# Performance work log

Hardware: AMD Instinct MI355X
Metric: run time of the kernel (lower is better)

Reference implementation:

```python
import jax, jax.numpy as jnp
import numpy as np

B, H, L = 8, 256, 16384

def setup_inputs() -> dict:
    key = jax.random.key(0)
    k1, k2, k3 = jax.random.split(key, 3)
    u = jax.random.normal(k1, (B, H, L), dtype=jnp.float32)
    # SSM convolution kernel (H, L); small scale to keep tanh unsaturated
    k = jax.random.normal(k2, (H, L), dtype=jnp.float32) * 0.02
    # D feedthrough parameter (H, H); forward only uses its diagonal via einsum 'hh,bhl->bhl'
    D = jax.random.normal(k3, (H, H), dtype=jnp.float32)
    return {"u": u, "k": k, "D": D}

def reference(u, k, D):
    # circular FFT convolution: y = ifft(fft(u) * fft(k)).real
    u_s = jnp.fft.fft(u, axis=-1)          # (B,H,L) complex64
    k_s = jnp.fft.fft(k, axis=-1)          # (H,L)   complex64
    y = jnp.fft.ifft(u_s * k_s[None], axis=-1).real
    # D feedthrough: einsum 'hh,bhl->bhl' uses only diag(D)
    y = y + jnp.einsum('hh,bhl->bhl', D, u)
    return jnp.tanh(y)
```

## Files before the change

### kernel.cpp

```cpp
#include <hip/hip_runtime.h>
#include <math.h>

#define FFT_N 16384
#define NT 512
#define RPT 32
#define B_DIM 8
#define H_DIM 256

#define REGION 2048
#define RW (REGION + (REGION >> 5))
#define PAD(x) ((x) + ((x) >> 5))

#define WAVE_LDS_FENCE() do {                                   \
    __builtin_amdgcn_sched_barrier(0);                          \
    asm volatile("s_waitcnt lgkmcnt(0)" ::: "memory");          \
    __builtin_amdgcn_sched_barrier(0);                          \
} while (0)

__device__ __forceinline__ float2 cmul(float2 a, float2 b) {
    return make_float2(a.x * b.x - a.y * b.y, a.x * b.y + a.y * b.x);
}
__device__ __forceinline__ float2 cadd(float2 a, float2 b) { return make_float2(a.x + b.x, a.y + b.y); }
__device__ __forceinline__ float2 csub(float2 a, float2 b) { return make_float2(a.x - b.x, a.y - b.y); }
__device__ __forceinline__ float2 mulnegi(float2 z) { return make_float2(z.y, -z.x); }
__device__ __forceinline__ float2 mulposi(float2 z) { return make_float2(-z.y, z.x); }

__device__ __forceinline__ void bfly4(float2& a, float2& b, float2& c, float2& d,
                                      float2 w1, float2 w2, float2 w3) {
    float2 apc = cadd(a, c), amc = csub(a, c);
    float2 bpd = cadd(b, d), bmd = csub(b, d);
    float2 nib = mulnegi(bmd);
    a = cadd(apc, bpd);
    b = cmul(csub(apc, bpd), w2);
    c = cmul(cadd(amc, nib), w1);
    d = cmul(csub(amc, nib), w3);
}
__device__ __forceinline__ void bfly4_nw(float2& a, float2& b, float2& c, float2& d) {
    float2 apc = cadd(a, c), amc = csub(a, c);
    float2 bpd = cadd(b, d), bmd = csub(b, d);
    float2 nib = mulnegi(bmd);
    a = cadd(apc, bpd);
    b = csub(apc, bpd);
    c = cadd(amc, nib);
    d = csub(amc, nib);
}
__device__ __forceinline__ void ibfly4(float2& a, float2& b, float2& c, float2& d,
                                       float2 w1t, float2 w2t) {
    float2 w1 = make_float2(w1t.x, -w1t.y);
    float2 w2 = make_float2(w2t.x, -w2t.y);
    float2 bt = cmul(b, w2), dt = cmul(d, w2);
    float2 A = cadd(a, bt), Bb = csub(a, bt);
    float2 C = cadd(c, dt), Dd = csub(c, dt);
    float2 Cw = cmul(C, w1);
    float2 Dw = mulposi(cmul(Dd, w1));
    a = cadd(A, Cw);  c = csub(A, Cw);
    b = cadd(Bb, Dw); d = csub(Bb, Dw);
}
__device__ __forceinline__ void ibfly4_nw(float2& a, float2& b, float2& c, float2& d) {
    float2 A = cadd(a, b), Bb = csub(a, b);
    float2 C = cadd(c, d), Dd = csub(c, d);
    float2 Dw = mulposi(Dd);
    a = cadd(A, C);  c = csub(A, C);
    b = cadd(Bb, Dw); d = csub(Bb, Dw);
}

__device__ __forceinline__ void fwd_g01(float2 r[RPT], int lp, const float2* __restrict__ tw) {
#pragma unroll
    for (int j0 = 0; j0 < 8; ++j0) {
        const int i = lp + NT * j0;
        bfly4(r[j0], r[j0 + 8], r[j0 + 16], r[j0 + 24], tw[i], tw[2 * i], tw[3 * i]);
    }
    {
        const int ie = lp * 4, io = (lp + NT) * 4;
        const float2 we1 = tw[ie], we2 = tw[2 * ie], we3 = tw[3 * ie];
        const float2 wo1 = tw[io], wo2 = tw[2 * io], wo3 = tw[3 * io];
#pragma unroll
        for (int m = 0; m < 8; ++m) {
            const int g = (m >> 1) * 8 + (m & 1);
            if (g & 1) bfly4(r[g], r[g + 2], r[g + 4], r[g + 6], wo1, wo2, wo3);
            else       bfly4(r[g], r[g + 2], r[g + 4], r[g + 6], we1, we2, we3);
        }
    }
}
__device__ __forceinline__ void inv_g01(float2 r[RPT], int lp, const float2* __restrict__ tw) {
    {
        const int ie = lp * 4, io = (lp + NT) * 4;
        const float2 we1 = tw[ie], we2 = tw[2 * ie];
        const float2 wo1 = tw[io], wo2 = tw[2 * io];
#pragma unroll
        for (int m = 0; m < 8; ++m) {
            const int g = (m >> 1) * 8 + (m & 1);
            if (g & 1) ibfly4(r[g], r[g + 2], r[g + 4], r[g + 6], wo1, wo2);
            else       ibfly4(r[g], r[g + 2], r[g + 4], r[g + 6], we1, we2);
        }
    }
#pragma unroll
    for (int j0 = 0; j0 < 8; ++j0) {
        const int i = lp + NT * j0;
        ibfly4(r[j0], r[j0 + 8], r[j0 + 16], r[j0 + 24], tw[i], tw[2 * i]);
    }
}


__device__ __forceinline__ void fwd_mid(float2 r[RPT], float* ldsx, float* ldsy,
                                        const int t, const int w, const int l,
                                        const float2* __restrict__ tw) {
#pragma unroll
    for (int j = 0; j < RPT; ++j) {
        const int e = t + NT * j;
        const int a = (e >> 11) * RW + PAD(e & 2047);
        ldsx[a] = r[j].x; ldsy[a] = r[j].y;
    }
    __syncthreads();
#pragma unroll
    for (int s = 0; s < 2; ++s)
#pragma unroll
        for (int jj = 0; jj < 16; ++jj) {
            const int a = w * RW + PAD(1024 * s + 64 * jj + l);
            r[16 * s + jj].x = ldsx[a];
            r[16 * s + jj].y = ldsy[a];
        }
#pragma unroll
    for (int j0 = 0; j0 < 4; ++j0) {
        const int i1 = 1024 * j0 + 16 * l;
        const float2 w1 = tw[i1], w2 = tw[2 * i1], w3 = tw[3 * i1];
#pragma unroll
        for (int s = 0; s < 2; ++s)
            bfly4(r[16 * s + j0], r[16 * s + j0 + 4], r[16 * s + j0 + 8], r[16 * s + j0 + 12], w1, w2, w3);
    }
    {
        const int i2 = 64 * l;
        const float2 w1 = tw[i2], w2 = tw[2 * i2], w3 = tw[3 * i2];
#pragma unroll
        for (int s = 0; s < 2; ++s)
#pragma unroll
            for (int g = 0; g < 4; ++g)
                bfly4(r[16 * s + 4 * g], r[16 * s + 4 * g + 1], r[16 * s + 4 * g + 2], r[16 * s + 4 * g + 3], w1, w2, w3);
    }
#pragma unroll
    for (int s = 0; s < 2; ++s)
#pragma unroll
        for (int jj = 0; jj < 16; ++jj) {
            const int a = w * RW + PAD(1024 * s + 64 * jj + l);
            ldsx[a] = r[16 * s + jj].x; ldsy[a] = r[16 * s + jj].y;
        }
    WAVE_LDS_FENCE();
    {
        const int lo = 64 * (l >> 2) + (l & 3);
#pragma unroll
        for (int s = 0; s < 2; ++s)
#pragma unroll
            for (int jj = 0; jj < 16; ++jj) {
                const int a = w * RW + PAD(1024 * s + lo + 4 * jj);
                r[16 * s + jj].x = ldsx[a]; r[16 * s + jj].y = ldsy[a];
            }
    }
#pragma unroll
    for (int j0 = 0; j0 < 4; ++j0) {
        const int i3 = 1024 * j0 + 256 * (l & 3);
        const float2 w1 = tw[i3], w2 = tw[2 * i3], w3 = tw[3 * i3];
#pragma unroll
        for (int s = 0; s < 2; ++s)
            bfly4(r[16 * s + j0], r[16 * s + j0 + 4], r[16 * s + j0 + 8], r[16 * s + j0 + 12], w1, w2, w3);
    }
    {
        const int i4 = 1024 * (l & 3);
        const float2 w1 = tw[i4], w2 = tw[2 * i4], w3 = tw[3 * i4];
#pragma unroll
        for (int s = 0; s < 2; ++s)
#pragma unroll
            for (int g = 0; g < 4; ++g)
                bfly4(r[16 * s + 4 * g], r[16 * s + 4 * g + 1], r[16 * s + 4 * g + 2], r[16 * s + 4 * g + 3], w1, w2, w3);
    }
    {
        const int lo = 64 * (l >> 2) + (l & 3);
#pragma unroll
        for (int s = 0; s < 2; ++s)
#pragma unroll
            for (int jj = 0; jj < 16; ++jj) {
                const int a = w * RW + PAD(1024 * s + lo + 4 * jj);
                ldsx[a] = r[16 * s + jj].x; ldsy[a] = r[16 * s + jj].y;
            }
    }
    WAVE_LDS_FENCE();
#pragma unroll
    for (int s = 0; s < 2; ++s)
#pragma unroll
        for (int jj = 0; jj < 16; ++jj) {
            const int a = w * RW + PAD(1024 * s + 16 * l + jj);
            r[16 * s + jj].x = ldsx[a]; r[16 * s + jj].y = ldsy[a];
        }
#pragma unroll
    for (int s = 0; s < 2; ++s)
#pragma unroll
        for (int g = 0; g < 4; ++g)
            bfly4_nw(r[16 * s + 4 * g], r[16 * s + 4 * g + 1], r[16 * s + 4 * g + 2], r[16 * s + 4 * g + 3]);
}

__device__ __forceinline__ void inv_mid(float2 r[RPT], float* ldsx, float* ldsy,
                                        const int t, const int w, const int l,
                                        const float2* __restrict__ tw) {
#pragma unroll
    for (int s = 0; s < 2; ++s)
#pragma unroll
        for (int g = 0; g < 4; ++g)
            ibfly4_nw(r[16 * s + 4 * g], r[16 * s + 4 * g + 1], r[16 * s + 4 * g + 2], r[16 * s + 4 * g + 3]);
#pragma unroll
    for (int s = 0; s < 2; ++s)
#pragma unroll
        for (int jj = 0; jj < 16; ++jj) {
            const int a = w * RW + PAD(1024 * s + 16 * l + jj);
            ldsx[a] = r[16 * s + jj].x; ldsy[a] = r[16 * s + jj].y;
        }
    WAVE_LDS_FENCE();
    {
        const int lo = 64 * (l >> 2) + (l & 3);
#pragma unroll
        for (int s = 0; s < 2; ++s)
#pragma unroll
            for (int jj = 0; jj < 16; ++jj) {
                const int a = w * RW + PAD(1024 * s + lo + 4 * jj);
                r[16 * s + jj].x = ldsx[a]; r[16 * s + jj].y = ldsy[a];
            }
    }
    {
        const int i4 = 1024 * (l & 3);
        const float2 w1 = tw[i4], w2 = tw[2 * i4];
#pragma unroll
        for (int s = 0; s < 2; ++s)
#pragma unroll
            for (int g = 0; g < 4; ++g)
                ibfly4(r[16 * s + 4 * g], r[16 * s + 4 * g + 1], r[16 * s + 4 * g + 2], r[16 * s + 4 * g + 3], w1, w2);
    }
#pragma unroll
    for (int j0 = 0; j0 < 4; ++j0) {
        const int i3 = 1024 * j0 + 256 * (l & 3);
        const float2 w1 = tw[i3], w2 = tw[2 * i3];
#pragma unroll
        for (int s = 0; s < 2; ++s)
            ibfly4(r[16 * s + j0], r[16 * s + j0 + 4], r[16 * s + j0 + 8], r[16 * s + j0 + 12], w1, w2);
    }
    {
        const int lo = 64 * (l >> 2) + (l & 3);
#pragma unroll
        for (int s = 0; s < 2; ++s)
#pragma unroll
            for (int jj = 0; jj < 16; ++jj) {
                const int a = w * RW + PAD(1024 * s + lo + 4 * jj);
                ldsx[a] = r[16 * s + jj].x; ldsy[a] = r[16 * s + jj].y;
            }
    }
    WAVE_LDS_FENCE();
#pragma unroll
    for (int s = 0; s < 2; ++s)
#pragma unroll
        for (int jj = 0; jj < 16; ++jj) {
            const int a = w * RW + PAD(1024 * s + 64 * jj + l);
            r[16 * s + jj].x = ldsx[a]; r[16 * s + jj].y = ldsy[a];
        }
    {
        const int i2 = 64 * l;
        const float2 w1 = tw[i2], w2 = tw[2 * i2];
#pragma unroll
        for (int s = 0; s < 2; ++s)
#pragma unroll
            for (int g = 0; g < 4; ++g)
                ibfly4(r[16 * s + 4 * g], r[16 * s + 4 * g + 1], r[16 * s + 4 * g + 2], r[16 * s + 4 * g + 3], w1, w2);
    }
#pragma unroll
    for (int j0 = 0; j0 < 4; ++j0) {
        const int i1 = 1024 * j0 + 16 * l;
        const float2 w1 = tw[i1], w2 = tw[2 * i1];
#pragma unroll
        for (int s = 0; s < 2; ++s)
            ibfly4(r[16 * s + j0], r[16 * s + j0 + 4], r[16 * s + j0 + 8], r[16 * s + j0 + 12], w1, w2);
    }
#pragma unroll
    for (int s = 0; s < 2; ++s)
#pragma unroll
        for (int jj = 0; jj < 16; ++jj) {
            const int a = w * RW + PAD(1024 * s + 64 * jj + l);
            ldsx[a] = r[16 * s + jj].x; ldsy[a] = r[16 * s + jj].y;
        }
    __syncthreads();
#pragma unroll
    for (int j = 0; j < RPT; ++j) {
        const int e = t + NT * j;
        const int a = (e >> 11) * RW + PAD(e & 2047);
        r[j].x = ldsx[a]; r[j].y = ldsy[a];
    }
}

__device__ __forceinline__ float ftanh(float x) {
    float e = __expf(2.0f * x);
    return 1.0f - 2.0f * __builtin_amdgcn_rcpf(e + 1.0f);
}

__global__ void twiddle_init(float2* __restrict__ tw) {
    int t = blockIdx.x * blockDim.x + threadIdx.x;
    if (t < FFT_N) {
        float ang = -2.0f * 3.14159265358979323846f * (float)t / (float)FFT_N;
        float sv, cv;
        sincosf(ang, &sv, &cv);
        tw[t] = make_float2(cv, sv);
    }
}

__global__ __launch_bounds__(NT)
__attribute__((amdgpu_waves_per_eu(2, 2)))
void kfft_kernel(const float* __restrict__ k,
                 const float* __restrict__ D,
                 const float2* __restrict__ tw,
                 float2* __restrict__ Kf) {
    __shared__ float ldsx[8 * RW];
    __shared__ float ldsy[8 * RW];
    const int h = blockIdx.x;
    const int t = threadIdx.x;
    const int w = t >> 6, l = t & 63;
    const float* krow = k + (size_t)h * FFT_N;
    float2 r[RPT];
#pragma unroll
    for (int j = 0; j < RPT; ++j) r[j] = make_float2(krow[t + NT * j], 0.f);
    if (t == 0) r[0].x += D[h * (H_DIM + 1)];
    fwd_g01(r, t, tw);
    fwd_mid(r, ldsx, ldsy, t, w, l, tw);
    float4* out4 = (float4*)(Kf + (size_t)h * FFT_N);
#pragma unroll
    for (int m = 0; m < 16; ++m)
        out4[16 * t + m] = make_float4(r[2 * m].x, r[2 * m].y, r[2 * m + 1].x, r[2 * m + 1].y);
}

__global__ __launch_bounds__(NT)
__attribute__((amdgpu_waves_per_eu(2, 2)))
void conv_kernel(const float* __restrict__ u,
                 const float2* __restrict__ tw,
                 const float2* __restrict__ Kf,
                 float* __restrict__ out) {
    __shared__ float ldsx[8 * RW];
    __shared__ float ldsy[8 * RW];
    const int raw = blockIdx.x;
    const int vb = ((raw & 7) << 7) + (raw >> 3);
    const int h = vb >> 2;
    const int p = vb & 3;
    const int t = threadIdx.x;
    const int w = t >> 6, l = t & 63;
    const size_t row0 = ((size_t)(2 * p) * H_DIM + h) * FFT_N;
    const size_t row1 = row0 + (size_t)H_DIM * FFT_N;
    const float* u0 = u + row0;
    const float* u1 = u + row1;

    float2 r[RPT];
#pragma unroll
    for (int j = 0; j < RPT; ++j) {
        const int n = t + NT * j;
        r[j] = make_float2(u0[n], u1[n]);
    }

    fwd_g01(r, t, tw);
    fwd_mid(r, ldsx, ldsy, t, w, l, tw);

    {
        const float4* kf4 = (const float4*)(Kf + (size_t)h * FFT_N);
        const float invN = 1.0f / (float)FFT_N;
#pragma unroll
        for (int m = 0; m < 16; ++m) {
            const float4 q = kf4[16 * t + m];
            const float2 z0 = r[2 * m], z1 = r[2 * m + 1];
            r[2 * m]     = make_float2((z0.x * q.x - z0.y * q.y) * invN,
                                       (z0.x * q.y + z0.y * q.x) * invN);
            r[2 * m + 1] = make_float2((z1.x * q.z - z1.y * q.w) * invN,
                                       (z1.x * q.w + z1.y * q.z) * invN);
        }
    }

    inv_mid(r, ldsx, ldsy, t, w, l, tw);
    inv_g01(r, t, tw);

    float* o0 = out + row0;
    float* o1 = out + row1;
#pragma unroll
    for (int j = 0; j < RPT; ++j) {
        const int n = t + NT * j;
        o0[n] = ftanh(r[j].x);
        o1[n] = ftanh(r[j].y);
    }
}

extern "C" void kernel_launch(void* const* d_in, const int* in_sizes, int n_in,
                              void* d_out, int out_size, void* d_ws, size_t ws_size,
                              hipStream_t stream) {
    const float* u = (const float*)d_in[0];
    const float* k = (const float*)d_in[1];
    const float* D = (const float*)d_in[2];
    float* out = (float*)d_out;

    float2* tw = (float2*)d_ws;
    float2* Kf = tw + FFT_N;

    twiddle_init<<<FFT_N / 256, 256, 0, stream>>>(tw);
    kfft_kernel<<<H_DIM, NT, 0, stream>>>(k, D, tw, Kf);
    conv_kernel<<<(B_DIM / 2) * H_DIM, NT, 0, stream>>>(u, tw, Kf, out);
}
```

Before: 199.3 us.

## Split 32-element per-thread FFT state into two 16-element halves to cut registers

Restructures the first two radix-4 stages and the per-wave middle stages so each thread processes two 16-element halves sequentially, spilling the first-stage results to LDS between halves. This lowers live register count and drops the forced waves_per_eu(2,2) attribute, aiming for higher occupancy or fewer spills. It adds extra LDS round trips (inverse first-stage input now read back from LDS) and an extra barrier before the output pass.

After: 224.1 us. 12.4% more time.

```diff
diff --git a/kernel.cpp b/kernel.cpp
--- a/kernel.cpp
+++ b/kernel.cpp
@@ -3,7 +3,6 @@
 
 #define FFT_N 16384
 #define NT 512
-#define RPT 32
 #define B_DIM 8
 #define H_DIM 256
 
@@ -64,230 +63,163 @@
     b = cadd(Bb, Dw); d = csub(Bb, Dw);
 }
 
-__device__ __forceinline__ void fwd_g01(float2 r[RPT], int lp, const float2* __restrict__ tw) {
-#pragma unroll
-    for (int j0 = 0; j0 < 8; ++j0) {
-        const int i = lp + NT * j0;
-        bfly4(r[j0], r[j0 + 8], r[j0 + 16], r[j0 + 24], tw[i], tw[2 * i], tw[3 * i]);
-    }
-    {
-        const int ie = lp * 4, io = (lp + NT) * 4;
-        const float2 we1 = tw[ie], we2 = tw[2 * ie], we3 = tw[3 * ie];
-        const float2 wo1 = tw[io], wo2 = tw[2 * io], wo3 = tw[3 * io];
-#pragma unroll
-        for (int m = 0; m < 8; ++m) {
-            const int g = (m >> 1) * 8 + (m & 1);
-            if (g & 1) bfly4(r[g], r[g + 2], r[g + 4], r[g + 6], wo1, wo2, wo3);
-            else       bfly4(r[g], r[g + 2], r[g + 4], r[g + 6], we1, we2, we3);
-        }
-    }
-}
-__device__ __forceinline__ void inv_g01(float2 r[RPT], int lp, const float2* __restrict__ tw) {
-    {
-        const int ie = lp * 4, io = (lp + NT) * 4;
-        const float2 we1 = tw[ie], we2 = tw[2 * ie];
-        const float2 wo1 = tw[io], wo2 = tw[2 * io];
-#pragma unroll
-        for (int m = 0; m < 8; ++m) {
-            const int g = (m >> 1) * 8 + (m & 1);
-            if (g & 1) ibfly4(r[g], r[g + 2], r[g + 4], r[g + 6], wo1, wo2);
-            else       ibfly4(r[g], r[g + 2], r[g + 4], r[g + 6], we1, we2);
-        }
-    }
-#pragma unroll
-    for (int j0 = 0; j0 < 8; ++j0) {
-        const int i = lp + NT * j0;
-        ibfly4(r[j0], r[j0 + 8], r[j0 + 16], r[j0 + 24], tw[i], tw[2 * i]);
-    }
-}
-
-
-__device__ __forceinline__ void fwd_mid(float2 r[RPT], float* ldsx, float* ldsy,
-                                        const int t, const int w, const int l,
-                                        const float2* __restrict__ tw) {
-#pragma unroll
-    for (int j = 0; j < RPT; ++j) {
-        const int e = t + NT * j;
-        const int a = (e >> 11) * RW + PAD(e & 2047);
-        ldsx[a] = r[j].x; ldsy[a] = r[j].y;
-    }
-    __syncthreads();
-#pragma unroll
-    for (int s = 0; s < 2; ++s)
-#pragma unroll
-        for (int jj = 0; jj < 16; ++jj) {
-            const int a = w * RW + PAD(1024 * s + 64 * jj + l);
-            r[16 * s + jj].x = ldsx[a];
-            r[16 * s + jj].y = ldsy[a];
-        }
+__device__ __forceinline__ void fwd_g01_half(float2 rh[16], const int t, const int par,
+                                             const float2* __restrict__ tw) {
+#pragma unroll
+    for (int m0 = 0; m0 < 4; ++m0) {
+        const int i = t + 512 * par + 1024 * m0;
+        bfly4(rh[m0], rh[m0 + 4], rh[m0 + 8], rh[m0 + 12], tw[i], tw[2 * i], tw[3 * i]);
+    }
+    {
+        const int ig = (t + 512 * par) * 4;
+        const float2 w1 = tw[ig], w2 = tw[2 * ig], w3 = tw[3 * ig];
+#pragma unroll
+        for (int a = 0; a < 4; ++a)
+            bfly4(rh[4 * a], rh[4 * a + 1], rh[4 * a + 2], rh[4 * a + 3], w1, w2, w3);
+    }
+}
+__device__ __forceinline__ void inv_g01_half(float2 rh[16], const int t, const int par,
+                                             const float2* __restrict__ tw) {
+    {
+        const int ig = (t + 512 * par) * 4;
+        const float2 w1 = tw[ig], w2 = tw[2 * ig];
+#pragma unroll
+        for (int a = 0; a < 4; ++a)
+            ibfly4(rh[4 * a], rh[4 * a + 1], rh[4 * a + 2], rh[4 * a + 3], w1, w2);
+    }
+#pragma unroll
+    for (int m0 = 0; m0 < 4; ++m0) {
+        const int i = t + 512 * par + 1024 * m0;
+        ibfly4(rh[m0], rh[m0 + 4], rh[m0 + 8], rh[m0 + 12], tw[i], tw[2 * i]);
+    }
+}
+
+__device__ __forceinline__ void fwd_mid_half(float2 rh[16], float* ldsx, float* ldsy,
+                                             const int w, const int l, const int s,
+                                             const float2* __restrict__ tw) {
+#pragma unroll
+    for (int jj = 0; jj < 16; ++jj) {
+        const int a = w * RW + PAD(1024 * s + 64 * jj + l);
+        rh[jj].x = ldsx[a]; rh[jj].y = ldsy[a];
+    }
 #pragma unroll
     for (int j0 = 0; j0 < 4; ++j0) {
         const int i1 = 1024 * j0 + 16 * l;
-        const float2 w1 = tw[i1], w2 = tw[2 * i1], w3 = tw[3 * i1];
-#pragma unroll
-        for (int s = 0; s < 2; ++s)
-            bfly4(r[16 * s + j0], r[16 * s + j0 + 4], r[16 * s + j0 + 8], r[16 * s + j0 + 12], w1, w2, w3);
+        bfly4(rh[j0], rh[j0 + 4], rh[j0 + 8], rh[j0 + 12], tw[i1], tw[2 * i1], tw[3 * i1]);
     }
     {
         const int i2 = 64 * l;
         const float2 w1 = tw[i2], w2 = tw[2 * i2], w3 = tw[3 * i2];
 #pragma unroll
-        for (int s = 0; s < 2; ++s)
-#pragma unroll
-            for (int g = 0; g < 4; ++g)
-                bfly4(r[16 * s + 4 * g], r[16 * s + 4 * g + 1], r[16 * s + 4 * g + 2], r[16 * s + 4 * g + 3], w1, w2, w3);
-    }
-#pragma unroll
-    for (int s = 0; s < 2; ++s)
+        for (int g = 0; g < 4; ++g)
+            bfly4(rh[4 * g], rh[4 * g + 1], rh[4 * g + 2], rh[4 * g + 3], w1, w2, w3);
+    }
+#pragma unroll
+    for (int jj = 0; jj < 16; ++jj) {
+        const int a = w * RW + PAD(1024 * s + 64 * jj + l);
+        ldsx[a] = rh[jj].x; ldsy[a] = rh[jj].y;
+    }
+    WAVE_LDS_FENCE();
+    {
+        const int lo = 64 * (l >> 2) + (l & 3);
 #pragma unroll
         for (int jj = 0; jj < 16; ++jj) {
-            const int a = w * RW + PAD(1024 * s + 64 * jj + l);
-            ldsx[a] = r[16 * s + jj].x; ldsy[a] = r[16 * s + jj].y;
-        }
-    WAVE_LDS_FENCE();
-    {
-        const int lo = 64 * (l >> 2) + (l & 3);
-#pragma unroll
-        for (int s = 0; s < 2; ++s)
-#pragma unroll
-            for (int jj = 0; jj < 16; ++jj) {
-                const int a = w * RW + PAD(1024 * s + lo + 4 * jj);
-                r[16 * s + jj].x = ldsx[a]; r[16 * s + jj].y = ldsy[a];
-            }
+            const int a = w * RW + PAD(1024 * s + lo + 4 * jj);
+            rh[jj].x = ldsx[a]; rh[jj].y = ldsy[a];
+        }
     }
 #pragma unroll
     for (int j0 = 0; j0 < 4; ++j0) {
         const int i3 = 1024 * j0 + 256 * (l & 3);
-        const float2 w1 = tw[i3], w2 = tw[2 * i3], w3 = tw[3 * i3];
-#pragma unroll
-        for (int s = 0; s < 2; ++s)
-            bfly4(r[16 * s + j0], r[16 * s + j0 + 4], r[16 * s + j0 + 8], r[16 * s + j0 + 12], w1, w2, w3);
+        bfly4(rh[j0], rh[j0 + 4], rh[j0 + 8], rh[j0 + 12], tw[i3], tw[2 * i3], tw[3 * i3]);
     }
     {
         const int i4 = 1024 * (l & 3);
         const float2 w1 = tw[i4], w2 = tw[2 * i4], w3 = tw[3 * i4];
 #pragma unroll
-        for (int s = 0; s < 2; ++s)
-#pragma unroll
-            for (int g = 0; g < 4; ++g)
-                bfly4(r[16 * s + 4 * g], r[16 * s + 4 * g + 1], r[16 * s + 4 * g + 2], r[16 * s + 4 * g + 3], w1, w2, w3);
+        for (int g = 0; g < 4; ++g)
+            bfly4(rh[4 * g], rh[4 * g + 1], rh[4 * g + 2], rh[4 * g + 3], w1, w2, w3);
     }
     {
         const int lo = 64 * (l >> 2) + (l & 3);
 #pragma unroll
-        for (int s = 0; s < 2; ++s)
-#pragma unroll
-            for (int jj = 0; jj < 16; ++jj) {
-                const int a = w * RW + PAD(1024 * s + lo + 4 * jj);
-                ldsx[a] = r[16 * s + jj].x; ldsy[a] = r[16 * s + jj].y;
-            }
+        for (int jj = 0; jj < 16; ++jj) {
+            const int a = w * RW + PAD(1024 * s + lo + 4 * jj);
+            ldsx[a] = rh[jj].x; ldsy[a] = rh[jj].y;
+        }
     }
     WAVE_LDS_FENCE();
 #pragma unroll
-    for (int s = 0; s < 2; ++s)
+    for (int jj = 0; jj < 16; ++jj) {
+        const int a = w * RW + PAD(1024 * s + 16 * l + jj);
+        rh[jj].x = ldsx[a]; rh[jj].y = ldsy[a];
+    }
+#pragma unroll
+    for (int g = 0; g < 4; ++g)
+        bfly4_nw(rh[4 * g], rh[4 * g + 1], rh[4 * g + 2], rh[4 * g + 3]);
+}
+__device__ __forceinline__ void inv_mid_half(float2 rh[16], float* ldsx, float* ldsy,
+                                             const int w, const int l, const int s,
+                                             const float2* __restrict__ tw) {
+#pragma unroll
+    for (int g = 0; g < 4; ++g)
+        ibfly4_nw(rh[4 * g], rh[4 * g + 1], rh[4 * g + 2], rh[4 * g + 3]);
+#pragma unroll
+    for (int jj = 0; jj < 16; ++jj) {
+        const int a = w * RW + PAD(1024 * s + 16 * l + jj);
+        ldsx[a] = rh[jj].x; ldsy[a] = rh[jj].y;
+    }
+    WAVE_LDS_FENCE();
+    {
+        const int lo = 64 * (l >> 2) + (l & 3);
 #pragma unroll
         for (int jj = 0; jj < 16; ++jj) {
-            const int a = w * RW + PAD(1024 * s + 16 * l + jj);
-            r[16 * s + jj].x = ldsx[a]; r[16 * s + jj].y = ldsy[a];
-        }
-#pragma unroll
-    for (int s = 0; s < 2; ++s)
-#pragma unroll
-        for (int g = 0; g < 4; ++g)
-            bfly4_nw(r[16 * s + 4 * g], r[16 * s + 4 * g + 1], r[16 * s + 4 * g + 2], r[16 * s + 4 * g + 3]);
-}
-
-__device__ __forceinline__ void inv_mid(float2 r[RPT], float* ldsx, float* ldsy,
-                                        const int t, const int w, const int l,
-                                        const float2* __restrict__ tw) {
-#pragma unroll
-    for (int s = 0; s < 2; ++s)
-#pragma unroll
-        for (int g = 0; g < 4; ++g)
-            ibfly4_nw(r[16 * s + 4 * g], r[16 * s + 4 * g + 1], r[16 * s + 4 * g + 2], r[16 * s + 4 * g + 3]);
-#pragma unroll
-    for (int s = 0; s < 2; ++s)
-#pragma unroll
-        for (int jj = 0; jj < 16; ++jj) {
-            const int a = w * RW + PAD(1024 * s + 16 * l + jj);
-            ldsx[a] = r[16 * s + jj].x; ldsy[a] = r[16 * s + jj].y;
-        }
-    WAVE_LDS_FENCE();
-    {
-        const int lo = 64 * (l >> 2) + (l & 3);
-#pragma unroll
-        for (int s = 0; s < 2; ++s)
-#pragma unroll
-            for (int jj = 0; jj < 16; ++jj) {
-                const int a = w * RW + PAD(1024 * s + lo + 4 * jj);
-                r[16 * s + jj].x = ldsx[a]; r[16 * s + jj].y = ldsy[a];
-            }
+            const int a = w * RW + PAD(1024 * s + lo + 4 * jj);
+            rh[jj].x = ldsx[a]; rh[jj].y = ldsy[a];
+        }
     }
     {
         const int i4 = 1024 * (l & 3);
         const float2 w1 = tw[i4], w2 = tw[2 * i4];
 #pragma unroll
-        for (int s = 0; s < 2; ++s)
-#pragma unroll
-            for (int g = 0; g < 4; ++g)
-                ibfly4(r[16 * s + 4 * g], r[16 * s + 4 * g + 1], r[16 * s + 4 * g + 2], r[16 * s + 4 * g + 3], w1, w2);
+        for (int g = 0; g < 4; ++g)
+            ibfly4(rh[4 * g], rh[4 * g + 1], rh[4 * g + 2], rh[4 * g + 3], w1, w2);
     }
 #pragma unroll
     for (int j0 = 0; j0 < 4; ++j0) {
         const int i3 = 1024 * j0 + 256 * (l & 3);
-        const float2 w1 = tw[i3], w2 = tw[2 * i3];
-#pragma unroll
-        for (int s = 0; s < 2; ++s)
-            ibfly4(r[16 * s + j0], r[16 * s + j0 + 4], r[16 * s + j0 + 8], r[16 * s + j0 + 12], w1, w2);
+        ibfly4(rh[j0], rh[j0 + 4], rh[j0 + 8], rh[j0 + 12], tw[i3], tw[2 * i3]);
     }
     {
         const int lo = 64 * (l >> 2) + (l & 3);
 #pragma unroll
-        for (int s = 0; s < 2; ++s)
-#pragma unroll
-            for (int jj = 0; jj < 16; ++jj) {
-                const int a = w * RW + PAD(1024 * s + lo + 4 * jj);
-                ldsx[a] = r[16 * s + jj].x; ldsy[a] = r[16 * s + jj].y;
-            }
+        for (int jj = 0; jj < 16; ++jj) {
+            const int a = w * RW + PAD(1024 * s + lo + 4 * jj);
+            ldsx[a] = rh[jj].x; ldsy[a] = rh[jj].y;
+        }
     }
     WAVE_LDS_FENCE();
 #pragma unroll
-    for (int s = 0; s < 2; ++s)
-#pragma unroll
-        for (int jj = 0; jj < 16; ++jj) {
-            const int a = w * RW + PAD(1024 * s + 64 * jj + l);
-            r[16 * s + jj].x = ldsx[a]; r[16 * s + jj].y = ldsy[a];
-        }
+    for (int jj = 0; jj < 16; ++jj) {
+        const int a = w * RW + PAD(1024 * s + 64 * jj + l);
+        rh[jj].x = ldsx[a]; rh[jj].y = ldsy[a];
+    }
     {
         const int i2 = 64 * l;
         const float2 w1 = tw[i2], w2 = tw[2 * i2];
 #pragma unroll
-        for (int s = 0; s < 2; ++s)
-#pragma unroll
-            for (int g = 0; g < 4; ++g)
-                ibfly4(r[16 * s + 4 * g], r[16 * s + 4 * g + 1], r[16 * s + 4 * g + 2], r[16 * s + 4 * g + 3], w1, w2);
+        for (int g = 0; g < 4; ++g)
+            ibfly4(rh[4 * g], rh[4 * g + 1], rh[4 * g + 2], rh[4 * g + 3], w1, w2);
     }
 #pragma unroll
     for (int j0 = 0; j0 < 4; ++j0) {
         const int i1 = 1024 * j0 + 16 * l;
-        const float2 w1 = tw[i1], w2 = tw[2 * i1];
-#pragma unroll
-        for (int s = 0; s < 2; ++s)
-            ibfly4(r[16 * s + j0], r[16 * s + j0 + 4], r[16 * s + j0 + 8], r[16 * s + j0 + 12], w1, w2);
-    }
-#pragma unroll
-    for (int s = 0; s < 2; ++s)
-#pragma unroll
-        for (int jj = 0; jj < 16; ++jj) {
-            const int a = w * RW + PAD(1024 * s + 64 * jj + l);
-            ldsx[a] = r[16 * s + jj].x; ldsy[a] = r[16 * s + jj].y;
-        }
-    __syncthreads();
-#pragma unroll
-    for (int j = 0; j < RPT; ++j) {
-        const int e = t + NT * j;
-        const int a = (e >> 11) * RW + PAD(e & 2047);
-        r[j].x = ldsx[a]; r[j].y = ldsy[a];
+        ibfly4(rh[j0], rh[j0 + 4], rh[j0 + 8], rh[j0 + 12], tw[i1], tw[2 * i1]);
+    }
+#pragma unroll
+    for (int jj = 0; jj < 16; ++jj) {
+        const int a = w * RW + PAD(1024 * s + 64 * jj + l);
+        ldsx[a] = rh[jj].x; ldsy[a] = rh[jj].y;
     }
 }
 
@@ -306,36 +238,49 @@
     }
 }
 
-__global__ __launch_bounds__(NT)
-__attribute__((amdgpu_waves_per_eu(2, 2)))
-void kfft_kernel(const float* __restrict__ k,
-                 const float* __restrict__ D,
-                 const float2* __restrict__ tw,
-                 float2* __restrict__ Kf) {
+__global__ __launch_bounds__(NT) void kfft_kernel(const float* __restrict__ k,
+                                                  const float* __restrict__ D,
+                                                  const float2* __restrict__ tw,
+                                                  float2* __restrict__ Kf) {
     __shared__ float ldsx[8 * RW];
     __shared__ float ldsy[8 * RW];
     const int h = blockIdx.x;
     const int t = threadIdx.x;
     const int w = t >> 6, l = t & 63;
     const float* krow = k + (size_t)h * FFT_N;
-    float2 r[RPT];
-#pragma unroll
-    for (int j = 0; j < RPT; ++j) r[j] = make_float2(krow[t + NT * j], 0.f);
-    if (t == 0) r[0].x += D[h * (H_DIM + 1)];
-    fwd_g01(r, t, tw);
-    fwd_mid(r, ldsx, ldsy, t, w, l, tw);
+    const float dh = D[h * (H_DIM + 1)];
+#pragma unroll
+    for (int par = 0; par < 2; ++par) {
+        float2 rh[16];
+#pragma unroll
+        for (int m = 0; m < 16; ++m)
+            rh[m] = make_float2(krow[t + 512 * par + 1024 * m], 0.f);
+        if (par == 0 && t == 0) rh[0].x += dh;
+        fwd_g01_half(rh, t, par, tw);
+#pragma unroll
+        for (int m = 0; m < 16; ++m) {
+            const int e = t + 512 * par + 1024 * m;
+            const int a = (e >> 11) * RW + PAD(e & 2047);
+            ldsx[a] = rh[m].x; ldsy[a] = rh[m].y;
+        }
+    }
+    __syncthreads();
     float4* out4 = (float4*)(Kf + (size_t)h * FFT_N);
 #pragma unroll
-    for (int m = 0; m < 16; ++m)
-        out4[16 * t + m] = make_float4(r[2 * m].x, r[2 * m].y, r[2 * m + 1].x, r[2 * m + 1].y);
-}
-
-__global__ __launch_bounds__(NT)
-__attribute__((amdgpu_waves_per_eu(2, 2)))
-void conv_kernel(const float* __restrict__ u,
-                 const float2* __restrict__ tw,
-                 const float2* __restrict__ Kf,
-                 float* __restrict__ out) {
+    for (int s = 0; s < 2; ++s) {
+        float2 rh[16];
+        fwd_mid_half(rh, ldsx, ldsy, w, l, s, tw);
+#pragma unroll
+        for (int q = 0; q < 8; ++q)
+            out4[16 * t + 8 * s + q] =
+                make_float4(rh[2 * q].x, rh[2 * q].y, rh[2 * q + 1].x, rh[2 * q + 1].y);
+    }
+}
+
+__global__ __launch_bounds__(NT) void conv_kernel(const float* __restrict__ u,
+                                                  const float2* __restrict__ tw,
+                                                  const float2* __restrict__ Kf,
+                                                  float* __restrict__ out) {
     __shared__ float ldsx[8 * RW];
     __shared__ float ldsy[8 * RW];
     const int raw = blockIdx.x;
@@ -349,40 +294,61 @@
     const float* u0 = u + row0;
     const float* u1 = u + row1;
 
-    float2 r[RPT];
-#pragma unroll
-    for (int j = 0; j < RPT; ++j) {
-        const int n = t + NT * j;
-        r[j] = make_float2(u0[n], u1[n]);
-    }
-
-    fwd_g01(r, t, tw);
-    fwd_mid(r, ldsx, ldsy, t, w, l, tw);
-
-    {
-        const float4* kf4 = (const float4*)(Kf + (size_t)h * FFT_N);
-        const float invN = 1.0f / (float)FFT_N;
-#pragma unroll
-        for (int m = 0; m < 16; ++m) {
-            const float4 q = kf4[16 * t + m];
-            const float2 z0 = r[2 * m], z1 = r[2 * m + 1];
-            r[2 * m]     = make_float2((z0.x * q.x - z0.y * q.y) * invN,
-                                       (z0.x * q.y + z0.y * q.x) * invN);
-            r[2 * m + 1] = make_float2((z1.x * q.z - z1.y * q.w) * invN,
-                                       (z1.x * q.w + z1.y * q.z) * invN);
-        }
-    }
-
-    inv_mid(r, ldsx, ldsy, t, w, l, tw);
-    inv_g01(r, t, tw);
+#pragma unroll
+    for (int par = 0; par < 2; ++par) {
+        float2 rh[16];
+#pragma unroll
+        for (int m = 0; m < 16; ++m) {
+            const int n = t + 512 * par + 1024 * m;
+            rh[m] = make_float2(u0[n], u1[n]);
+        }
+        fwd_g01_half(rh, t, par, tw);
+#pragma unroll
+        for (int m = 0; m < 16; ++m) {
+            const int e = t + 512 * par + 1024 * m;
+            const int a = (e >> 11) * RW + PAD(e & 2047);
+            ldsx[a] = rh[m].x; ldsy[a] = rh[m].y;
+        }
+    }
+    __syncthreads();
+
+    const float4* kf4 = (const float4*)(Kf + (size_t)h * FFT_N);
+    const float invN = 1.0f / (float)FFT_N;
+#pragma unroll
+    for (int s = 0; s < 2; ++s) {
+        float2 rh[16];
+        fwd_mid_half(rh, ldsx, ldsy, w, l, s, tw);
+#pragma unroll
+        for (int q = 0; q < 8; ++q) {
+            const float4 kw = kf4[16 * t + 8 * s + q];
+            const float2 z0 = rh[2 * q], z1 = rh[2 * q + 1];
+            rh[2 * q]     = make_float2((z0.x * kw.x - z0.y * kw.y) * invN,
+                                        (z0.x * kw.y + z0.y * kw.x) * invN);
+            rh[2 * q + 1] = make_float2((z1.x * kw.z - z1.y * kw.w) * invN,
+                                        (z1.x * kw.w + z1.y * kw.z) * invN);
+        }
+        inv_mid_half(rh, ldsx, ldsy, w, l, s, tw);
+    }
+    __syncthreads();
 
     float* o0 = out + row0;
     float* o1 = out + row1;
 #pragma unroll
-    for (int j = 0; j < RPT; ++j) {
-        const int n = t + NT * j;
-        o0[n] = ftanh(r[j].x);
-        o1[n] = ftanh(r[j].y);
+    for (int par = 0; par < 2; ++par) {
+        float2 rh[16];
+#pragma unroll
+        for (int m = 0; m < 16; ++m) {
+            const int e = t + 512 * par + 1024 * m;
+            const int a = (e >> 11) * RW + PAD(e & 2047);
+            rh[m].x = ldsx[a]; rh[m].y = ldsy[a];
+        }
+        inv_g01_half(rh, t, par, tw);
+#pragma unroll
+        for (int m = 0; m < 16; ++m) {
+            const int n = t + 512 * par + 1024 * m;
+            o0[n] = ftanh(rh[m].x);
+            o1[n] = ftanh(rh[m].y);
+        }
     }
 }
 
```
